# Optimization experiments

Hardware: AMD Instinct MI355X
Metric: run time of the kernel (lower is better)

Reference implementation:

```python
import jax, jax.numpy as jnp
import numpy as np

B, L_DEC, L_ENC = 4, 1024, 1024
D_MODEL, D_INNER, N_HEAD, D_K, D_V = 512, 256, 8, 64, 64
TEMP = D_K ** 0.5
EPS = 1e-6


def _layernorm(x, g, b):
    mu = jnp.mean(x, axis=-1, keepdims=True)
    var = jnp.mean(jnp.square(x - mu), axis=-1, keepdims=True)
    return (x - mu) * jax.lax.rsqrt(var + EPS) * g + b


def _mha(x_q, x_kv, Wq, Wk, Wv, Wfc, ln_g, ln_b, mask):
    # Faithful to source: only the query input is layer-normed; k/v use raw x_kv.
    resid = x_q
    qn = _layernorm(x_q, ln_g, ln_b)
    # Stacked per-head projections: Wq/Wk/Wv are [H, d_k, d_model]
    q = jnp.einsum('bld,hkd->bhlk', qn, Wq) / TEMP   # [B,H,Lq,dk]
    k = jnp.einsum('bld,hkd->bhlk', x_kv, Wk)        # [B,H,Lk,dk]
    v = jnp.einsum('bld,hkd->bhlk', x_kv, Wv)        # [B,H,Lk,dv]
    scores = jnp.einsum('bhqd,bhkd->bhqk', q, k)     # [B,H,Lq,Lk]
    if mask is not None:
        scores = jnp.where(mask[:, None, :, :] == 0, -jnp.inf, scores)
    attn = jax.nn.softmax(scores, axis=-1)
    out = jnp.einsum('bhqk,bhkd->bhqd', attn, v)     # [B,H,Lq,dv]
    Bq, H, Lq, dv = out.shape
    out = out.transpose(0, 2, 1, 3).reshape(Bq, Lq, H * dv)
    return out @ Wfc.T + resid


def _ffn(x, W1, b1, W2, b2, ln_g, ln_b):
    resid = x
    h = _layernorm(x, ln_g, ln_b)
    h = jax.nn.relu(h @ W1.T + b1) @ W2.T + b2
    return h + resid


def setup_inputs() -> dict:
    key = jax.random.key(0)
    ks = jax.random.split(key, 20)
    s = 0.02
    dec_input = jax.random.normal(ks[0], (B, L_DEC, D_MODEL), jnp.float32)
    enc_output = jax.random.normal(ks[1], (B, L_ENC, D_MODEL), jnp.float32)
    slf_attn_mask = jnp.tril(jnp.ones((1, L_DEC, L_DEC), jnp.int32))  # causal
    p = {}
    for i, pre in enumerate(['slf', 'enc']):
        base = 2 + i * 4
        p[f'{pre}_Wq'] = jax.random.normal(ks[base], (N_HEAD, D_K, D_MODEL), jnp.float32) * s
        p[f'{pre}_Wk'] = jax.random.normal(ks[base + 1], (N_HEAD, D_K, D_MODEL), jnp.float32) * s
        p[f'{pre}_Wv'] = jax.random.normal(ks[base + 2], (N_HEAD, D_V, D_MODEL), jnp.float32) * s
        p[f'{pre}_Wfc'] = jax.random.normal(ks[base + 3], (D_MODEL, N_HEAD * D_V), jnp.float32) * s
        p[f'{pre}_ln_g'] = jnp.ones((D_MODEL,), jnp.float32)
        p[f'{pre}_ln_b'] = jnp.zeros((D_MODEL,), jnp.float32)
    p['ffn_W1'] = jax.random.normal(ks[10], (D_INNER, D_MODEL), jnp.float32) * s
    p['ffn_b1'] = jnp.zeros((D_INNER,), jnp.float32)
    p['ffn_W2'] = jax.random.normal(ks[11], (D_MODEL, D_INNER), jnp.float32) * s
    p['ffn_b2'] = jnp.zeros((D_MODEL,), jnp.float32)
    p['ffn_ln_g'] = jnp.ones((D_MODEL,), jnp.float32)
    p['ffn_ln_b'] = jnp.zeros((D_MODEL,), jnp.float32)
    return {'dec_input': dec_input, 'enc_output': enc_output,
            'slf_attn_mask': slf_attn_mask, **p}


def reference(dec_input, enc_output,
              slf_Wq, slf_Wk, slf_Wv, slf_Wfc, slf_ln_g, slf_ln_b,
              enc_Wq, enc_Wk, enc_Wv, enc_Wfc, enc_ln_g, enc_ln_b,
              ffn_W1, ffn_b1, ffn_W2, ffn_b2, ffn_ln_g, ffn_ln_b,
              slf_attn_mask):
    x = _mha(dec_input, dec_input, slf_Wq, slf_Wk, slf_Wv, slf_Wfc,
             slf_ln_g, slf_ln_b, slf_attn_mask)
    x = _mha(x, enc_output, enc_Wq, enc_Wk, enc_Wv, enc_Wfc,
             enc_ln_g, enc_ln_b, None)
    x = _ffn(x, ffn_W1, ffn_b1, ffn_W2, ffn_b2, ffn_ln_g, ffn_ln_b)
    return x
```

## Files before the change

### kernel.cpp

```cpp
#include <hip/hip_runtime.h>
#include <hip/hip_bf16.h>
#include <math.h>

#define DMODEL 512
#define NHEAD  8
#define DHEAD  64

typedef __attribute__((ext_vector_type(8))) short bf16x8;
typedef __attribute__((ext_vector_type(4))) float f32x4;
typedef __attribute__((ext_vector_type(4))) short short4v;

static __device__ inline short f2bf(float f) {
    __hip_bfloat16 h = __float2bfloat16(f);
    return *reinterpret_cast<short*>(&h);
}

#define GLOAD_LDS16(gp, lp)                                                      \
    __builtin_amdgcn_global_load_lds(                                            \
        (const __attribute__((address_space(1))) unsigned int*)(gp),             \
        (__attribute__((address_space(3))) unsigned int*)(lp), 16, 0, 0)

struct CvtArgs {
    const float* src[12];
    short*       dst[12];
    int          n[12];
};

__global__ __launch_bounds__(256) void cvt_kernel(CvtArgs args) {
    int t = blockIdx.y;
    int idx = (blockIdx.x * 256 + threadIdx.x) * 8;
    if (idx >= args.n[t]) return;
    const float* s = args.src[t] + idx;
    float4 a = *(const float4*)s;
    float4 b = *(const float4*)(s + 4);
    bf16x8 o;
    o[0] = f2bf(a.x); o[1] = f2bf(a.y); o[2] = f2bf(a.z); o[3] = f2bf(a.w);
    o[4] = f2bf(b.x); o[5] = f2bf(b.y); o[6] = f2bf(b.z); o[7] = f2bf(b.w);
    *(bf16x8*)(args.dst[t] + idx) = o;
}

__global__ __launch_bounds__(256) void ln_kernel(const float* __restrict__ X,
                                                 const float* __restrict__ gam,
                                                 const float* __restrict__ bet,
                                                 short* __restrict__ Y) {
    int row = blockIdx.x * 4 + (threadIdx.x >> 6);
    int tid = threadIdx.x & 63;
    const float* x = X + (size_t)row * DMODEL;
    float4 a = *(const float4*)(x + tid * 4);
    float4 b = *(const float4*)(x + 256 + tid * 4);
    float sum = a.x + a.y + a.z + a.w + b.x + b.y + b.z + b.w;
    float sq  = a.x*a.x + a.y*a.y + a.z*a.z + a.w*a.w
              + b.x*b.x + b.y*b.y + b.z*b.z + b.w*b.w;
#pragma unroll
    for (int off = 1; off < 64; off <<= 1) {
        sum += __shfl_xor(sum, off);
        sq  += __shfl_xor(sq, off);
    }
    float mu  = sum * (1.0f / DMODEL);
    float var = sq * (1.0f / DMODEL) - mu * mu;
    float r   = rsqrtf(var + 1e-6f);

    float4 g1 = *(const float4*)(gam + tid * 4);
    float4 c1 = *(const float4*)(bet + tid * 4);
    float4 g2 = *(const float4*)(gam + 256 + tid * 4);
    float4 c2 = *(const float4*)(bet + 256 + tid * 4);
    short4v y1, y2;
    y1.x = f2bf((a.x - mu) * r * g1.x + c1.x);
    y1.y = f2bf((a.y - mu) * r * g1.y + c1.y);
    y1.z = f2bf((a.z - mu) * r * g1.z + c1.z);
    y1.w = f2bf((a.w - mu) * r * g1.w + c1.w);
    y2.x = f2bf((b.x - mu) * r * g2.x + c2.x);
    y2.y = f2bf((b.y - mu) * r * g2.y + c2.y);
    y2.z = f2bf((b.z - mu) * r * g2.z + c2.z);
    y2.w = f2bf((b.w - mu) * r * g2.w + c2.w);
    short* y = Y + (size_t)row * DMODEL;
    *(short4v*)(y + tid * 4)       = y1;
    *(short4v*)(y + 256 + tid * 4) = y2;
}

struct GJobs {
    const short* A[3];
    const short* W[3];
    const float* bias[3];
    const float* resid[3];
    void*        C[3];
    int M[3], N[3], K[3];
    float scale[3];
    int relu[3], obf[3], nblk[3];
};

__global__ __launch_bounds__(256) void gemm_bf16(GJobs jb) {
    __shared__ short As[64 * 64];
    __shared__ short Bs[64 * 64];

    int bid = blockIdx.x, j = 0;
    while (j < 2 && bid >= jb.nblk[j]) { bid -= jb.nblk[j]; ++j; }
    const short* __restrict__ A = jb.A[j];
    const short* __restrict__ W = jb.W[j];
    const int N = jb.N[j], K = jb.K[j];
    const int nbx = N >> 6;
    const int tn = (bid % nbx) * 64;
    const int tm = (bid / nbx) * 64;

    const int tid  = threadIdx.x;
    const int w    = tid >> 6;
    const int l    = tid & 63;
    const int lq   = l & 15;
    const int g    = l >> 4;
    const int wm   = (w >> 1) * 32;
    const int wn   = (w & 1) * 32;
    const int lrow = l >> 3;
    const int lsl  = l & 7;

    f32x4 acc[2][2];
#pragma unroll
    for (int i = 0; i < 2; ++i)
#pragma unroll
        for (int jj = 0; jj < 2; ++jj)
            acc[i][jj] = (f32x4){0.f, 0.f, 0.f, 0.f};

#pragma unroll 1
    for (int k0 = 0; k0 < K; k0 += 64) {
        __syncthreads();
#pragma unroll
        for (int i = 0; i < 2; ++i) {
            int row = i * 32 + w * 8 + lrow;
            int slot = lsl ^ (row & 7);
            GLOAD_LDS16(A + (size_t)(tm + row) * K + k0 + slot * 8,
                        As + i * 2048 + w * 512);
            GLOAD_LDS16(W + (size_t)(tn + row) * K + k0 + slot * 8,
                        Bs + i * 2048 + w * 512);
        }
        __syncthreads();

#pragma unroll
        for (int ks = 0; ks < 2; ++ks) {
            const int sl = ((ks * 4 + g) ^ (lq & 7)) * 8;
            bf16x8 af[2], bfv[2];
#pragma unroll
            for (int i = 0; i < 2; ++i) {
                af[i]  = *(const bf16x8*)&As[(wm + i * 16 + lq) * 64 + sl];
                bfv[i] = *(const bf16x8*)&Bs[(wn + i * 16 + lq) * 64 + sl];
            }
#pragma unroll
            for (int i = 0; i < 2; ++i)
#pragma unroll
                for (int jj = 0; jj < 2; ++jj)
                    acc[i][jj] = __builtin_amdgcn_mfma_f32_16x16x32_bf16(
                        af[i], bfv[jj], acc[i][jj], 0, 0, 0);
        }
    }

    const float* bias  = jb.bias[j];
    const float* resid = jb.resid[j];
    const float scale  = jb.scale[j];
    const int relu = jb.relu[j], obf = jb.obf[j];
#pragma unroll
    for (int i = 0; i < 2; ++i) {
#pragma unroll
        for (int r = 0; r < 4; ++r) {
            int row = tm + wm + i * 16 + g * 4 + r;
#pragma unroll
            for (int jj = 0; jj < 2; ++jj) {
                int col = tn + wn + jj * 16 + lq;
                float v = acc[i][jj][r] * scale;
                if (bias)  v += bias[col];
                if (resid) v += resid[(size_t)row * N + col];
                if (relu)  v = fmaxf(v, 0.f);
                if (obf) ((short*)jb.C[j])[(size_t)row * N + col] = f2bf(v);
                else     ((float*)jb.C[j])[(size_t)row * N + col] = v;
            }
        }
    }
}

__global__ __launch_bounds__(256) void attn_mfma_kernel(
        const short* __restrict__ Q, const short* __restrict__ K,
        const short* __restrict__ V, short* __restrict__ O,
        int Lq, int Lk, int causal, int qs, int kvs) {
    __shared__ short Kt[64 * 64];
    __shared__ short Vt[64][72];
    __shared__ short Pb[4][16][72];

    const int tid  = threadIdx.x;
    const int wave = tid >> 6;
    const int lane = tid & 63;
    const int lq   = lane & 15;
    const int g    = lane >> 4;
    const int bh   = blockIdx.y;
    const int b = bh >> 3, h = bh & 7;
    const int NQT = Lq >> 4;
    int gw = blockIdx.x * 4 + wave;
    const int qt = (gw & 1) ? (NQT - 1 - (gw >> 1)) : (gw >> 1);
    const int q0 = qt * 16;
    const float NEG = -__builtin_inff();

    size_t qoff = (size_t)(b * Lq + q0 + lq) * qs + h * DHEAD;
    bf16x8 qf0 = *(const bf16x8*)(Q + qoff + g * 8);
    bf16x8 qf1 = *(const bf16x8*)(Q + qoff + 32 + g * 8);

    f32x4 o[4] = {{0,0,0,0},{0,0,0,0},{0,0,0,0},{0,0,0,0}};
    f32x4 lacc = {0.f, 0.f, 0.f, 0.f};

    bf16x8 ones;
    {
        short ov = (lq == 0) ? (short)0x3F80 : (short)0;
#pragma unroll
        for (int i = 0; i < 8; ++i) ones[i] = ov;
    }

    const int nkt = causal ? ((qt >> 2) + 1) : (Lk >> 6);
    const int lrow = lane >> 3;
    const int lsl  = lane & 7;
    const int va = tid & 31;
    const int vd = (tid >> 5) * 8;

#pragma unroll 1
    for (int kt = 0; kt < nkt; ++kt) {
        __syncthreads();
#pragma unroll
        for (int i = 0; i < 2; ++i) {
            int row = i * 32 + wave * 8 + lrow;
            int slot = lsl ^ (row & 7);
            GLOAD_LDS16(K + (size_t)(b * Lk + kt * 64 + row) * kvs + h * DHEAD + slot * 8,
                        Kt + i * 2048 + wave * 512);
        }
        {
            size_t gb = (size_t)(b * Lk + kt * 64 + 2 * va) * kvs + h * DHEAD + vd;
            bf16x8 v0 = *(const bf16x8*)(V + gb);
            bf16x8 v1 = *(const bf16x8*)(V + gb + kvs);
#pragma unroll
            for (int i = 0; i < 8; ++i) {
                unsigned p = (unsigned short)v0[i] | ((unsigned)(unsigned short)v1[i] << 16);
                *(unsigned*)&Vt[vd + i][2 * va] = p;
            }
        }
        __syncthreads();

        f32x4 s[4];
#pragma unroll
        for (int sub = 0; sub < 4; ++sub) {
            int rr = sub * 16 + lq;
            const int sl0 = ((0 + g) ^ (lq & 7)) * 8;
            const int sl1 = ((4 + g) ^ (lq & 7)) * 8;
            bf16x8 kf0 = *(const bf16x8*)&Kt[rr * 64 + sl0];
            bf16x8 kf1 = *(const bf16x8*)&Kt[rr * 64 + sl1];
            f32x4 a = {0.f, 0.f, 0.f, 0.f};
            a = __builtin_amdgcn_mfma_f32_16x16x32_bf16(kf0, qf0, a, 0, 0, 0);
            a = __builtin_amdgcn_mfma_f32_16x16x32_bf16(kf1, qf1, a, 0, 0, 0);
            s[sub] = a;
        }
        if (causal && kt == nkt - 1) {
            int qg = q0 + lq;
#pragma unroll
            for (int sub = 0; sub < 4; ++sub) {
#pragma unroll
                for (int r = 0; r < 4; ++r) {
                    int kg = kt * 64 + sub * 16 + g * 4 + r;
                    if (kg > qg) s[sub][r] = NEG;
                }
            }
        }

#pragma unroll
        for (int sub = 0; sub < 4; ++sub) {
            short4v p4;
            p4.x = f2bf(__expf(fminf(s[sub][0], 60.f)));
            p4.y = f2bf(__expf(fminf(s[sub][1], 60.f)));
            p4.z = f2bf(__expf(fminf(s[sub][2], 60.f)));
            p4.w = f2bf(__expf(fminf(s[sub][3], 60.f)));
            *(short4v*)&Pb[wave][lq][sub * 16 + g * 4] = p4;
        }
        bf16x8 pf0 = *(const bf16x8*)&Pb[wave][lq][g * 8];
        bf16x8 pf1 = *(const bf16x8*)&Pb[wave][lq][32 + g * 8];

#pragma unroll
        for (int dc = 0; dc < 4; ++dc) {
            bf16x8 vf0 = *(const bf16x8*)&Vt[dc * 16 + lq][g * 8];
            bf16x8 vf1 = *(const bf16x8*)&Vt[dc * 16 + lq][32 + g * 8];
            o[dc] = __builtin_amdgcn_mfma_f32_16x16x32_bf16(pf0, vf0, o[dc], 0, 0, 0);
            o[dc] = __builtin_amdgcn_mfma_f32_16x16x32_bf16(pf1, vf1, o[dc], 0, 0, 0);
        }
        lacc = __builtin_amdgcn_mfma_f32_16x16x32_bf16(pf0, ones, lacc, 0, 0, 0);
        lacc = __builtin_amdgcn_mfma_f32_16x16x32_bf16(pf1, ones, lacc, 0, 0, 0);
    }

#pragma unroll
    for (int r = 0; r < 4; ++r) {
        float lr = __shfl(lacc[r], g << 4);
        float inv = 1.f / lr;
        size_t ob = (size_t)(b * Lq + q0 + g * 4 + r) * qs + h * DHEAD + lq;
        O[ob + 0]  = f2bf(o[0][r] * inv);
        O[ob + 16] = f2bf(o[1][r] * inv);
        O[ob + 32] = f2bf(o[2][r] * inv);
        O[ob + 48] = f2bf(o[3][r] * inv);
    }
}

static void launch_gemm(GJobs& jb, int njobs, hipStream_t stream) {
    int total = 0;
    for (int i = 0; i < 3; ++i) { if (i >= njobs) jb.nblk[i] = 0; total += jb.nblk[i]; }
    gemm_bf16<<<total, 256, 0, stream>>>(jb);
}

extern "C" void kernel_launch(void* const* d_in, const int* in_sizes, int n_in,
                              void* d_out, int out_size, void* d_ws, size_t ws_size,
                              hipStream_t stream) {
    const float* dec       = (const float*)d_in[0];
    const float* enc       = (const float*)d_in[1];
    const float* slf_Wq    = (const float*)d_in[3];
    const float* slf_Wk    = (const float*)d_in[4];
    const float* slf_Wv    = (const float*)d_in[5];
    const float* slf_Wfc   = (const float*)d_in[6];
    const float* slf_ln_g  = (const float*)d_in[7];
    const float* slf_ln_b  = (const float*)d_in[8];
    const float* enc_Wq    = (const float*)d_in[9];
    const float* enc_Wk    = (const float*)d_in[10];
    const float* enc_Wv    = (const float*)d_in[11];
    const float* enc_Wfc   = (const float*)d_in[12];
    const float* enc_ln_g  = (const float*)d_in[13];
    const float* enc_ln_b  = (const float*)d_in[14];
    const float* ffn_W1    = (const float*)d_in[15];
    const float* ffn_b1    = (const float*)d_in[16];
    const float* ffn_W2    = (const float*)d_in[17];
    const float* ffn_b2    = (const float*)d_in[18];
    const float* ffn_ln_g  = (const float*)d_in[19];
    const float* ffn_ln_b  = (const float*)d_in[20];
    float* out = (float*)d_out;

    const int Bb = 4, L = 1024, M = Bb * L;
    const size_t NE = (size_t)M * DMODEL;
    const int WQN = NHEAD * DHEAD * DMODEL;
    float* ws = (float*)d_ws;
    float* x1 = ws;
    float* x2 = ws + NE;
    short* kv16e = (short*)x2;
    short* sb = (short*)(ws + 2 * NE);
    short* dec16 = sb;               sb += NE;
    short* enc16 = sb;               sb += NE;
    short* qn16  = sb;               sb += NE;
    short* q16   = sb;               sb += NE;
    short* ao16  = sb;               sb += NE;
    short* kv16  = sb;               sb += 2 * NE;
    short* h16   = sb;               sb += NE / 2;
    short* wq_s  = sb;               sb += WQN;
    short* wkv_s = sb;               sb += 2 * WQN;
    short* wfc_s = sb;               sb += WQN;
    short* wq_e  = sb;               sb += WQN;
    short* wkv_e = sb;               sb += 2 * WQN;
    short* wfc_e = sb;               sb += WQN;
    short* w1_16 = sb;               sb += 256 * DMODEL;
    short* w2_16 = sb;               sb += DMODEL * 256;

    CvtArgs ca;
    ca.src[0] = dec;     ca.dst[0] = dec16;         ca.n[0] = (int)NE;
    ca.src[1] = enc;     ca.dst[1] = enc16;         ca.n[1] = (int)NE;
    ca.src[2] = slf_Wq;  ca.dst[2] = wq_s;          ca.n[2] = WQN;
    ca.src[3] = slf_Wk;  ca.dst[3] = wkv_s;         ca.n[3] = WQN;
    ca.src[4] = slf_Wv;  ca.dst[4] = wkv_s + WQN;   ca.n[4] = WQN;
    ca.src[5] = slf_Wfc; ca.dst[5] = wfc_s;         ca.n[5] = WQN;
    ca.src[6] = enc_Wq;  ca.dst[6] = wq_e;          ca.n[6] = WQN;
    ca.src[7] = enc_Wk;  ca.dst[7] = wkv_e;         ca.n[7] = WQN;
    ca.src[8] = enc_Wv;  ca.dst[8] = wkv_e + WQN;   ca.n[8] = WQN;
    ca.src[9] = enc_Wfc; ca.dst[9] = wfc_e;         ca.n[9] = WQN;
    ca.src[10] = ffn_W1; ca.dst[10] = w1_16;        ca.n[10] = 256 * DMODEL;
    ca.src[11] = ffn_W2; ca.dst[11] = w2_16;        ca.n[11] = DMODEL * 256;
    cvt_kernel<<<dim3(1024, 12), 256, 0, stream>>>(ca);

    dim3 attn_grid(L / 64, Bb * NHEAD);
    const int NB512  = (M / 64) * (512 / 64);
    const int NB1024 = (M / 64) * (1024 / 64);
    const int NB256  = (M / 64) * (256 / 64);

    ln_kernel<<<M / 4, 256, 0, stream>>>(dec, slf_ln_g, slf_ln_b, qn16);
    {
        GJobs jb = {};
        jb.A[0] = qn16;  jb.W[0] = wq_s;  jb.C[0] = q16;
        jb.M[0] = M; jb.N[0] = 512;  jb.K[0] = 512; jb.scale[0] = 0.125f;
        jb.obf[0] = 1; jb.nblk[0] = NB512;
        jb.A[1] = dec16; jb.W[1] = wkv_s; jb.C[1] = kv16;
        jb.M[1] = M; jb.N[1] = 1024; jb.K[1] = 512; jb.scale[1] = 1.f;
        jb.obf[1] = 1; jb.nblk[1] = NB1024;
        jb.A[2] = enc16; jb.W[2] = wkv_e; jb.C[2] = kv16e;
        jb.M[2] = M; jb.N[2] = 1024; jb.K[2] = 512; jb.scale[2] = 1.f;
        jb.obf[2] = 1; jb.nblk[2] = NB1024;
        launch_gemm(jb, 3, stream);
    }
    attn_mfma_kernel<<<attn_grid, 256, 0, stream>>>(q16, kv16, kv16 + 512, ao16,
                                                    L, L, 1, DMODEL, 1024);
    {
        GJobs jb = {};
        jb.A[0] = ao16; jb.W[0] = wfc_s; jb.resid[0] = dec; jb.C[0] = x1;
        jb.M[0] = M; jb.N[0] = 512; jb.K[0] = 512; jb.scale[0] = 1.f;
        jb.obf[0] = 0; jb.nblk[0] = NB512;
        launch_gemm(jb, 1, stream);
    }

    ln_kernel<<<M / 4, 256, 0, stream>>>(x1, enc_ln_g, enc_ln_b, qn16);
    {
        GJobs jb = {};
        jb.A[0] = qn16; jb.W[0] = wq_e; jb.C[0] = q16;
        jb.M[0] = M; jb.N[0] = 512; jb.K[0] = 512; jb.scale[0] = 0.125f;
        jb.obf[0] = 1; jb.nblk[0] = NB512;
        launch_gemm(jb, 1, stream);
    }
    attn_mfma_kernel<<<attn_grid, 256, 0, stream>>>(q16, kv16e, kv16e + 512, ao16,
                                                    L, L, 0, DMODEL, 1024);
    {
        GJobs jb = {};
        jb.A[0] = ao16; jb.W[0] = wfc_e; jb.resid[0] = x1; jb.C[0] = x2;
        jb.M[0] = M; jb.N[0] = 512; jb.K[0] = 512; jb.scale[0] = 1.f;
        jb.obf[0] = 0; jb.nblk[0] = NB512;
        launch_gemm(jb, 1, stream);
    }

    ln_kernel<<<M / 4, 256, 0, stream>>>(x2, ffn_ln_g, ffn_ln_b, qn16);
    {
        GJobs jb = {};
        jb.A[0] = qn16; jb.W[0] = w1_16; jb.bias[0] = ffn_b1; jb.C[0] = h16;
        jb.M[0] = M; jb.N[0] = 256; jb.K[0] = 512; jb.scale[0] = 1.f;
        jb.relu[0] = 1; jb.obf[0] = 1; jb.nblk[0] = NB256;
        launch_gemm(jb, 1, stream);
    }
    {
        GJobs jb = {};
        jb.A[0] = h16; jb.W[0] = w2_16; jb.bias[0] = ffn_b2; jb.resid[0] = x2;
        jb.C[0] = out;
        jb.M[0] = M; jb.N[0] = 512; jb.K[0] = 256; jb.scale[0] = 1.f;
        jb.obf[0] = 0; jb.nblk[0] = NB512;
        launch_gemm(jb, 1, stream);
    }
}
```

Before: 251.2 us.

## Double-buffer GEMM tiles, fold activation casts into LayerNorm, rebalance causal attention bands

The GEMM gets two LDS buffers so the next K tile's global-to-LDS load is issued while the current tile is multiplied, and one barrier per iteration is dropped. The fp32-to-bf16 conversion of dec_input and enc_output moves out of the conversion kernel and into the first LayerNorm pass, which already reads dec, so one pass over dec is saved and the conversion kernel shrinks to weights only. Causal attention now gives each block one contiguous band of four query tiles, with the band order reversed for half of the batch-heads to balance load across blocks. The risks are LDS doubling, correctness depending on the async LDS loads being waited on at the barrier, and coarser load balancing in attention.

Result: no change. 255.6 us (+1.7%).

```diff
diff --git a/kernel.cpp b/kernel.cpp
--- a/kernel.cpp
+++ b/kernel.cpp
@@ -21,9 +21,9 @@
         (__attribute__((address_space(3))) unsigned int*)(lp), 16, 0, 0)
 
 struct CvtArgs {
-    const float* src[12];
-    short*       dst[12];
-    int          n[12];
+    const float* src[10];
+    short*       dst[10];
+    int          n[10];
 };
 
 __global__ __launch_bounds__(256) void cvt_kernel(CvtArgs args) {
@@ -42,7 +42,11 @@
 __global__ __launch_bounds__(256) void ln_kernel(const float* __restrict__ X,
                                                  const float* __restrict__ gam,
                                                  const float* __restrict__ bet,
-                                                 short* __restrict__ Y) {
+                                                 short* __restrict__ Y,
+                                                 const float* __restrict__ C1s,
+                                                 short* __restrict__ C1d,
+                                                 const float* __restrict__ C2s,
+                                                 short* __restrict__ C2d) {
     int row = blockIdx.x * 4 + (threadIdx.x >> 6);
     int tid = threadIdx.x & 63;
     const float* x = X + (size_t)row * DMODEL;
@@ -76,6 +80,26 @@
     short* y = Y + (size_t)row * DMODEL;
     *(short4v*)(y + tid * 4)       = y1;
     *(short4v*)(y + 256 + tid * 4) = y2;
+
+    if (C1s) {
+        short4v d1, d2;
+        d1.x = f2bf(a.x); d1.y = f2bf(a.y); d1.z = f2bf(a.z); d1.w = f2bf(a.w);
+        d2.x = f2bf(b.x); d2.y = f2bf(b.y); d2.z = f2bf(b.z); d2.w = f2bf(b.w);
+        short* d = C1d + (size_t)row * DMODEL;
+        *(short4v*)(d + tid * 4)       = d1;
+        *(short4v*)(d + 256 + tid * 4) = d2;
+    }
+    if (C2s) {
+        const float* e = C2s + (size_t)row * DMODEL;
+        float4 ea = *(const float4*)(e + tid * 4);
+        float4 eb = *(const float4*)(e + 256 + tid * 4);
+        short4v d1, d2;
+        d1.x = f2bf(ea.x); d1.y = f2bf(ea.y); d1.z = f2bf(ea.z); d1.w = f2bf(ea.w);
+        d2.x = f2bf(eb.x); d2.y = f2bf(eb.y); d2.z = f2bf(eb.z); d2.w = f2bf(eb.w);
+        short* d = C2d + (size_t)row * DMODEL;
+        *(short4v*)(d + tid * 4)       = d1;
+        *(short4v*)(d + 256 + tid * 4) = d2;
+    }
 }
 
 struct GJobs {
@@ -90,8 +114,8 @@
 };
 
 __global__ __launch_bounds__(256) void gemm_bf16(GJobs jb) {
-    __shared__ short As[64 * 64];
-    __shared__ short Bs[64 * 64];
+    __shared__ short As[2][64 * 64];
+    __shared__ short Bs[2][64 * 64];
 
     int bid = blockIdx.x, j = 0;
     while (j < 2 && bid >= jb.nblk[j]) { bid -= jb.nblk[j]; ++j; }
@@ -119,28 +143,33 @@
         for (int jj = 0; jj < 2; ++jj)
             acc[i][jj] = (f32x4){0.f, 0.f, 0.f, 0.f};
 
+#define GSTAGE(buf, koff)                                                        \
+    do {                                                                         \
+        _Pragma("unroll")                                                        \
+        for (int i_ = 0; i_ < 2; ++i_) {                                         \
+            int row_ = i_ * 32 + w * 8 + lrow;                                   \
+            int slot_ = lsl ^ (row_ & 7);                                        \
+            GLOAD_LDS16(A + (size_t)(tm + row_) * K + (koff) + slot_ * 8,        \
+                        As[buf] + i_ * 2048 + w * 512);                          \
+            GLOAD_LDS16(W + (size_t)(tn + row_) * K + (koff) + slot_ * 8,        \
+                        Bs[buf] + i_ * 2048 + w * 512);                          \
+        }                                                                        \
+    } while (0)
+
+    GSTAGE(0, 0);
+    int buf = 0;
 #pragma unroll 1
-    for (int k0 = 0; k0 < K; k0 += 64) {
+    for (int k0 = 0; k0 < K; k0 += 64, buf ^= 1) {
         __syncthreads();
-#pragma unroll
-        for (int i = 0; i < 2; ++i) {
-            int row = i * 32 + w * 8 + lrow;
-            int slot = lsl ^ (row & 7);
-            GLOAD_LDS16(A + (size_t)(tm + row) * K + k0 + slot * 8,
-                        As + i * 2048 + w * 512);
-            GLOAD_LDS16(W + (size_t)(tn + row) * K + k0 + slot * 8,
-                        Bs + i * 2048 + w * 512);
-        }
-        __syncthreads();
-
+        if (k0 + 64 < K) GSTAGE(buf ^ 1, k0 + 64);
 #pragma unroll
         for (int ks = 0; ks < 2; ++ks) {
             const int sl = ((ks * 4 + g) ^ (lq & 7)) * 8;
             bf16x8 af[2], bfv[2];
 #pragma unroll
             for (int i = 0; i < 2; ++i) {
-                af[i]  = *(const bf16x8*)&As[(wm + i * 16 + lq) * 64 + sl];
-                bfv[i] = *(const bf16x8*)&Bs[(wn + i * 16 + lq) * 64 + sl];
+                af[i]  = *(const bf16x8*)&As[buf][(wm + i * 16 + lq) * 64 + sl];
+                bfv[i] = *(const bf16x8*)&Bs[buf][(wn + i * 16 + lq) * 64 + sl];
             }
 #pragma unroll
             for (int i = 0; i < 2; ++i)
@@ -150,6 +179,7 @@
                         af[i], bfv[jj], acc[i][jj], 0, 0, 0);
         }
     }
+#undef GSTAGE
 
     const float* bias  = jb.bias[j];
     const float* resid = jb.resid[j];
@@ -189,9 +219,9 @@
     const int g    = lane >> 4;
     const int bh   = blockIdx.y;
     const int b = bh >> 3, h = bh & 7;
-    const int NQT = Lq >> 4;
-    int gw = blockIdx.x * 4 + wave;
-    const int qt = (gw & 1) ? (NQT - 1 - (gw >> 1)) : (gw >> 1);
+    const int band = causal ? ((bh < 16) ? (int)blockIdx.x : (15 - (int)blockIdx.x))
+                            : (int)blockIdx.x;
+    const int qt = band * 4 + wave;
     const int q0 = qt * 16;
     const float NEG = -__builtin_inff();
 
@@ -209,7 +239,7 @@
         for (int i = 0; i < 8; ++i) ones[i] = ov;
     }
 
-    const int nkt = causal ? ((qt >> 2) + 1) : (Lk >> 6);
+    const int nkt = causal ? (band + 1) : (Lk >> 6);
     const int lrow = lane >> 3;
     const int lsl  = lane & 7;
     const int va = tid & 31;
@@ -353,26 +383,25 @@
     short* w2_16 = sb;               sb += DMODEL * 256;
 
     CvtArgs ca;
-    ca.src[0] = dec;     ca.dst[0] = dec16;         ca.n[0] = (int)NE;
-    ca.src[1] = enc;     ca.dst[1] = enc16;         ca.n[1] = (int)NE;
-    ca.src[2] = slf_Wq;  ca.dst[2] = wq_s;          ca.n[2] = WQN;
-    ca.src[3] = slf_Wk;  ca.dst[3] = wkv_s;         ca.n[3] = WQN;
-    ca.src[4] = slf_Wv;  ca.dst[4] = wkv_s + WQN;   ca.n[4] = WQN;
-    ca.src[5] = slf_Wfc; ca.dst[5] = wfc_s;         ca.n[5] = WQN;
-    ca.src[6] = enc_Wq;  ca.dst[6] = wq_e;          ca.n[6] = WQN;
-    ca.src[7] = enc_Wk;  ca.dst[7] = wkv_e;         ca.n[7] = WQN;
-    ca.src[8] = enc_Wv;  ca.dst[8] = wkv_e + WQN;   ca.n[8] = WQN;
-    ca.src[9] = enc_Wfc; ca.dst[9] = wfc_e;         ca.n[9] = WQN;
-    ca.src[10] = ffn_W1; ca.dst[10] = w1_16;        ca.n[10] = 256 * DMODEL;
-    ca.src[11] = ffn_W2; ca.dst[11] = w2_16;        ca.n[11] = DMODEL * 256;
-    cvt_kernel<<<dim3(1024, 12), 256, 0, stream>>>(ca);
+    ca.src[0] = slf_Wq;  ca.dst[0] = wq_s;          ca.n[0] = WQN;
+    ca.src[1] = slf_Wk;  ca.dst[1] = wkv_s;         ca.n[1] = WQN;
+    ca.src[2] = slf_Wv;  ca.dst[2] = wkv_s + WQN;   ca.n[2] = WQN;
+    ca.src[3] = slf_Wfc; ca.dst[3] = wfc_s;         ca.n[3] = WQN;
+    ca.src[4] = enc_Wq;  ca.dst[4] = wq_e;          ca.n[4] = WQN;
+    ca.src[5] = enc_Wk;  ca.dst[5] = wkv_e;         ca.n[5] = WQN;
+    ca.src[6] = enc_Wv;  ca.dst[6] = wkv_e + WQN;   ca.n[6] = WQN;
+    ca.src[7] = enc_Wfc; ca.dst[7] = wfc_e;         ca.n[7] = WQN;
+    ca.src[8] = ffn_W1;  ca.dst[8] = w1_16;         ca.n[8] = 256 * DMODEL;
+    ca.src[9] = ffn_W2;  ca.dst[9] = w2_16;         ca.n[9] = DMODEL * 256;
+    cvt_kernel<<<dim3(128, 10), 256, 0, stream>>>(ca);
 
     dim3 attn_grid(L / 64, Bb * NHEAD);
     const int NB512  = (M / 64) * (512 / 64);
     const int NB1024 = (M / 64) * (1024 / 64);
     const int NB256  = (M / 64) * (256 / 64);
 
-    ln_kernel<<<M / 4, 256, 0, stream>>>(dec, slf_ln_g, slf_ln_b, qn16);
+    ln_kernel<<<M / 4, 256, 0, stream>>>(dec, slf_ln_g, slf_ln_b, qn16,
+                                         dec, dec16, enc, enc16);
     {
         GJobs jb = {};
         jb.A[0] = qn16;  jb.W[0] = wq_s;  jb.C[0] = q16;
@@ -396,7 +425,8 @@
         launch_gemm(jb, 1, stream);
     }
 
-    ln_kernel<<<M / 4, 256, 0, stream>>>(x1, enc_ln_g, enc_ln_b, qn16);
+    ln_kernel<<<M / 4, 256, 0, stream>>>(x1, enc_ln_g, enc_ln_b, qn16,
+                                         nullptr, nullptr, nullptr, nullptr);
     {
         GJobs jb = {};
         jb.A[0] = qn16; jb.W[0] = wq_e; jb.C[0] = q16;
@@ -414,7 +444,8 @@
         launch_gemm(jb, 1, stream);
     }
 
-    ln_kernel<<<M / 4, 256, 0, stream>>>(x2, ffn_ln_g, ffn_ln_b, qn16);
+    ln_kernel<<<M / 4, 256, 0, stream>>>(x2, ffn_ln_g, ffn_ln_b, qn16,
+                                         nullptr, nullptr, nullptr, nullptr);
     {
         GJobs jb = {};
         jb.A[0] = qn16; jb.W[0] = w1_16; jb.bias[0] = ffn_b1; jb.C[0] = h16;
```
